# Optimization experiments

Measured on AMD Instinct MI355X. Metric: run time of the kernel, lower is better.

Reference implementation:

```python
import jax, jax.numpy as jnp
import numpy as np

N = 20000
E = 640000
IN_CH = 256
HID = 128
OUT_CH = 64
HEADS = 8
C1 = HID // HEADS   # 16 per-head dim, layer 1 (concat)
C2 = OUT_CH         # 64 per-head dim, layer 2 (head mean)
NEG_SLOPE = 0.2


def gat_conv(x, edge_index, W, a_src, a_dst, b, concat):
    """PyG GATConv (no self loops, eval mode / no dropout).
    W: [F_in, H*C], a_src/a_dst: [H, C], b: [H*C] or [C]."""
    H, C = a_src.shape
    h = (x @ W).reshape(-1, H, C)                      # [N, H, C]
    s_src = jnp.einsum('nhc,hc->nh', h, a_src)         # [N, H]
    s_dst = jnp.einsum('nhc,hc->nh', h, a_dst)         # [N, H]
    src, dst = edge_index[0], edge_index[1]
    e = jax.nn.leaky_relu(s_src[src] + s_dst[dst], NEG_SLOPE)  # [E, H]
    # segment softmax over incoming edges of each destination node
    m = jax.ops.segment_max(e, dst, num_segments=N)    # [N, H] (-inf for isolated)
    p = jnp.exp(e - m[dst])                            # [E, H]
    z = jax.ops.segment_sum(p, dst, num_segments=N)    # [N, H]
    alpha = p / z[dst]                                 # [E, H]
    out = jax.ops.segment_sum(h[src] * alpha[..., None], dst, num_segments=N)  # [N,H,C]
    out = out.reshape(-1, H * C) if concat else out.mean(axis=1)
    return out + b


def hetero_layer(x, edge_indices, Ws, a_srcs, a_dsts, bs, concat):
    # HeteroConv(aggr='mean') over edge types targeting 'user'
    outs = [gat_conv(x, edge_indices[t], Ws[t], a_srcs[t], a_dsts[t], bs[t], concat)
            for t in range(len(edge_indices))]
    return sum(outs) / len(outs)


def setup_inputs() -> dict:
    key = jax.random.key(0)
    ks = jax.random.split(key, 16)
    g = 0.1
    return {
        'x': jax.random.normal(ks[0], (N, IN_CH), dtype=jnp.float32),
        'edge_index_a': jax.random.randint(ks[1], (2, E), 0, N, dtype=jnp.int32).astype(jnp.int64),
        'edge_index_b': jax.random.randint(ks[2], (2, E), 0, N, dtype=jnp.int32).astype(jnp.int64),
        # layer 1 params, stacked over 2 edge types
        'W1': jax.random.normal(ks[3], (2, IN_CH, HEADS * C1), dtype=jnp.float32) * g,
        'a1_src': jax.random.normal(ks[4], (2, HEADS, C1), dtype=jnp.float32) * g,
        'a1_dst': jax.random.normal(ks[5], (2, HEADS, C1), dtype=jnp.float32) * g,
        'b1': jnp.zeros((2, HEADS * C1), dtype=jnp.float32),
        # layer 2 params
        'W2': jax.random.normal(ks[6], (2, HID, HEADS * C2), dtype=jnp.float32) * g,
        'a2_src': jax.random.normal(ks[7], (2, HEADS, C2), dtype=jnp.float32) * g,
        'a2_dst': jax.random.normal(ks[8], (2, HEADS, C2), dtype=jnp.float32) * g,
        'b2': jnp.zeros((2, C2), dtype=jnp.float32),
        # classifier
        'Wc1': jax.random.normal(ks[9], (OUT_CH, 32), dtype=jnp.float32) * g,
        'bc1': jnp.zeros((32,), dtype=jnp.float32),
        'Wc2': jax.random.normal(ks[10], (32, 2), dtype=jnp.float32) * g,
        'bc2': jnp.zeros((2,), dtype=jnp.float32),
    }


def reference(x, edge_index_a, edge_index_b, W1, a1_src, a1_dst, b1,
              W2, a2_src, a2_dst, b2, Wc1, bc1, Wc2, bc2):
    eis = [edge_index_a, edge_index_b]
    h = hetero_layer(x, eis, W1, a1_src, a1_dst, b1, concat=True)   # [N, 128]
    h = jax.nn.elu(h)  # (dropout is identity in eval mode)
    h = hetero_layer(h, eis, W2, a2_src, a2_dst, b2, concat=False)  # [N, 64]
    h = jax.nn.elu(h)
    logits = jax.nn.relu(h @ Wc1 + bc1) @ Wc2 + bc2                 # [N, 2]
    return logits
```

## Files before the change

kernel.cpp:

```cpp
#include <hip/hip_runtime.h>
#include <hip/hip_bf16.h>
#include <math.h>

#define NN 20000
#define EE 640000
#define NB 157
#define BCAP 5120
#define NBLK 160
#define CHNK 4000

typedef float v2f __attribute__((ext_vector_type(2)));
typedef __attribute__((ext_vector_type(8))) short bf16x8;
typedef __attribute__((ext_vector_type(4))) float f32x4;

__device__ __forceinline__ void wave_fence() {
  __builtin_amdgcn_wave_barrier();
  asm volatile("s_waitcnt lgkmcnt(0)" ::: "memory");
  __builtin_amdgcn_wave_barrier();
}

__device__ __forceinline__ unsigned pack_bf2(float a, float b) {
  __hip_bfloat162 h2 = __float22bfloat162_rn(make_float2(a, b));
  return *(unsigned*)&h2;
}
__device__ __forceinline__ float2 unpack_bf2(unsigned v) {
  float2 r;
  unsigned lo = v << 16, hi = v & 0xffff0000u;
  r.x = __uint_as_float(lo);
  r.y = __uint_as_float(hi);
  return r;
}

__global__ __launch_bounds__(256) void bin_k(const int* __restrict__ ea,
                                             const int* __restrict__ eb,
                                             int* __restrict__ gcnt,
                                             int* __restrict__ bbuf) {
  int t = blockIdx.y;
  const int* ei = t ? eb : ea;
  int tid = threadIdx.x;
  __shared__ int lh[NB], lbase[NB];
  if (tid < NB) lh[tid] = 0;
  __syncthreads();
  int e0 = blockIdx.x * CHNK;
  int e1 = min(e0 + CHNK, EE);
  int myb[16], myr[16], myv[16];
#pragma unroll
  for (int i = 0; i < 16; ++i) {
    int e = e0 + tid + i * 256;
    if (e < e1) {
      int s = ei[e], d = ei[EE + e];
      int b = d >> 7;
      myb[i] = b;
      myv[i] = (s << 7) | (d & 127);
      myr[i] = atomicAdd(&lh[b], 1);
    } else {
      myb[i] = -1;
    }
  }
  __syncthreads();
  if (tid < NB) {
    int c = lh[tid];
    lbase[tid] = c ? atomicAdd(&gcnt[t * NB + tid], c) : 0;
  }
  __syncthreads();
#pragma unroll
  for (int i = 0; i < 16; ++i) {
    int b = myb[i];
    if (b >= 0) {
      int pos = lbase[b] + myr[i];
      if (pos < BCAP) bbuf[((size_t)t * NB + b) * BCAP + pos] = myv[i];
    }
  }
}

__global__ __launch_bounds__(512) void bscan_k(const int* __restrict__ gcnt,
                                               int* __restrict__ bstart) {
  __shared__ int buf[512];
  int tid = threadIdx.x;
  int t = tid >> 8, b = tid & 255;
  int val = (b < NB) ? gcnt[t * NB + b] : 0;
  buf[tid] = val;
  __syncthreads();
  for (int s = 1; s < 256; s <<= 1) {
    int x = ((tid & 255) >= s) ? buf[tid - s] : 0;
    __syncthreads();
    buf[tid] += x;
    __syncthreads();
  }
  if (b < NB) bstart[t * NB + b] = buf[tid] - val;
}

__global__ __launch_bounds__(256) void build_k(const int* __restrict__ gcnt,
                                               const int* __restrict__ bstart,
                                               const int* __restrict__ bbuf,
                                               int* __restrict__ rowptr,
                                               int* __restrict__ csr) {
  int b = blockIdx.x, t = blockIdx.y;
  int cnt = gcnt[t * NB + b];
  int start = bstart[t * NB + b];
  int n0 = b << 7;
  int nlocal = min(128, NN - n0);
  int tid = threadIdx.x;
  __shared__ int arr[128], lcur[128];
  if (tid < 128) arr[tid] = 0;
  __syncthreads();
  const int* ebuf = bbuf + ((size_t)t * NB + b) * BCAP;
  for (int i = tid; i < cnt; i += 256) atomicAdd(&arr[ebuf[i] & 127], 1);
  __syncthreads();
  int deg = (tid < 128) ? arr[tid] : 0;
  for (int s = 1; s < 128; s <<= 1) {
    int x = (tid < 128 && tid >= s) ? arr[tid - s] : 0;
    __syncthreads();
    if (tid < 128) arr[tid] += x;
    __syncthreads();
  }
  if (tid < nlocal) {
    int incl = arr[tid];
    rowptr[t * (NN + 1) + n0 + tid + 1] = start + incl;
    lcur[tid] = start + incl - deg;
  }
  if (b == 0 && tid == 0) rowptr[t * (NN + 1)] = 0;
  __syncthreads();
  for (int i = tid; i < cnt; i += 256) {
    int v = ebuf[i];
    int pos = atomicAdd(&lcur[v & 127], 1);
    csr[(size_t)t * EE + pos] = v >> 7;
  }
}

template <int NT, int BM, int BN, int BK, int TM, int TN>
__global__ __launch_bounds__(NT) void sgemm_k(const float* __restrict__ A,
                                              const float* __restrict__ B,
                                              float* __restrict__ C, int M, int N, int K,
                                              long long Abs, long long Bbs, long long Cbs,
                                              unsigned* __restrict__ Cb, long long Cbb) {
  A += blockIdx.z * Abs; B += blockIdx.z * Bbs;
  if (C) C += blockIdx.z * Cbs;
  if (Cb) Cb += blockIdx.z * Cbb;
  const int bm = blockIdx.x * BM, bn = blockIdx.y * BN;
  __shared__ float As[BK][BM + 4];
  __shared__ float Bs[BK][BN + 4];
  int tid = threadIdx.x;
  constexpr int TX = BN / TN;
  int tx = tid % TX, ty = tid / TX;
  float acc[TM][TN] = {};
  for (int k0 = 0; k0 < K; k0 += BK) {
#pragma unroll
    for (int i = 0; i < (BM * BK) / (NT * 4); ++i) {
      int idx = tid + i * NT;
      int row = idx / (BK / 4), kq = idx % (BK / 4);
      float4 v = make_float4(0.f, 0.f, 0.f, 0.f);
      int gr = bm + row;
      if (gr < M) v = *(const float4*)&A[(size_t)gr * K + k0 + kq * 4];
      As[kq * 4 + 0][row] = v.x; As[kq * 4 + 1][row] = v.y;
      As[kq * 4 + 2][row] = v.z; As[kq * 4 + 3][row] = v.w;
    }
#pragma unroll
    for (int i = 0; i < (BK * BN) / (NT * 4); ++i) {
      int idx = tid + i * NT;
      int row = idx / (BN / 4), cq = idx % (BN / 4);
      *(float4*)&Bs[row][cq * 4] = *(const float4*)&B[(size_t)(k0 + row) * N + bn + cq * 4];
    }
    __syncthreads();
#pragma unroll
    for (int k = 0; k < BK; ++k) {
      float a[TM], b[TN];
#pragma unroll
      for (int i = 0; i < TM; i += 4) *(float4*)&a[i] = *(float4*)&As[k][ty * TM + i];
#pragma unroll
      for (int j = 0; j < TN; j += 4) *(float4*)&b[j] = *(float4*)&Bs[k][tx * TN + j];
#pragma unroll
      for (int i = 0; i < TM; ++i)
#pragma unroll
        for (int j = 0; j < TN; ++j) acc[i][j] += a[i] * b[j];
    }
    __syncthreads();
  }
#pragma unroll
  for (int i = 0; i < TM; ++i) {
    int gr = bm + ty * TM + i;
    if (gr < M) {
      if (C) {
#pragma unroll
        for (int j = 0; j < TN; j += 4)
          *(float4*)&C[(size_t)gr * N + bn + tx * TN + j] = *(float4*)&acc[i][j];
      }
      if (Cb) {
#pragma unroll
        for (int j = 0; j < TN; j += 2)
          Cb[(size_t)gr * (N >> 1) + ((bn + tx * TN + j) >> 1)] = pack_bf2(acc[i][j], acc[i][j + 1]);
      }
    }
  }
}

__global__ void scoreb_k(const unsigned* __restrict__ hb, const float* __restrict__ as_,
                         const float* __restrict__ ad_, float* __restrict__ ss,
                         float* __restrict__ sd) {
  int idx = blockIdx.x * 256 + threadIdx.x;
  if (idx >= 2 * NN * 8) return;
  int t = idx / (NN * 8), r = idx % (NN * 8), n = r / 8, hh = r % 8;
  const unsigned* hrow = hb + (size_t)t * NN * 64 + (size_t)n * 64 + hh * 8;
  const float* a1 = as_ + t * 128 + hh * 16;
  const float* a2 = ad_ + t * 128 + hh * 16;
  uint4 u0 = *(const uint4*)&hrow[0];
  uint4 u1 = *(const uint4*)&hrow[4];
  unsigned uu[8] = {u0.x, u0.y, u0.z, u0.w, u1.x, u1.y, u1.z, u1.w};
  float s1 = 0.f, s2 = 0.f;
#pragma unroll
  for (int q = 0; q < 8; ++q) {
    float2 f = unpack_bf2(uu[q]);
    s1 += f.x * a1[2 * q] + f.y * a1[2 * q + 1];
    s2 += f.x * a2[2 * q] + f.y * a2[2 * q + 1];
  }
  ss[idx] = s1; sd[idx] = s2;
}

__device__ __forceinline__ float lrelu(float v) { return v > 0.f ? v : 0.2f * v; }

__global__ __launch_bounds__(256) void aggw1_k(const int* __restrict__ rowptr,
                                               const int* __restrict__ csr,
                                               const float* __restrict__ ssrc,
                                               const float* __restrict__ sdst,
                                               const unsigned* __restrict__ hb,
                                               float* __restrict__ out) {
  int t = blockIdx.y;
  rowptr += t * (NN + 1); csr += (size_t)t * EE;
  ssrc += (size_t)t * NN * 8; sdst += (size_t)t * NN * 8;
  hb += (size_t)t * NN * 64; out += (size_t)t * NN * 128;
  int tid = threadIdx.x, w = tid >> 6, lane = tid & 63;
  int n = blockIdx.x * 4 + w;
  int row = rowptr[n], end = rowptr[n + 1];
  __shared__ __align__(16) int sidx[4][64];
  __shared__ __align__(16) float sexp[4][64][8];
  float4 sda = *(const float4*)&sdst[(size_t)n * 8];
  float4 sdb = *(const float4*)&sdst[(size_t)n * 8 + 4];
  float za_x = 0.f, za_y = 0.f, za_z = 0.f, za_w = 0.f;
  float zb_x = 0.f, zb_y = 0.f, zb_z = 0.f, zb_w = 0.f;
  int hme = lane >> 3;
  unsigned lane4 = lane << 2;
  const char* hbc = (const char*)hb;
  v2f acc = {0.f, 0.f};
  for (int base = row; base < end; base += 64) {
    int cnt = min(64, end - base);
    if (lane < cnt) {
      int s = csr[base + lane];
      sidx[w][lane] = s << 8;
      float4 pa = *(const float4*)&ssrc[(size_t)s * 8];
      float4 pb = *(const float4*)&ssrc[(size_t)s * 8 + 4];
      float4 ea, eb;
      ea.x = __expf(lrelu(pa.x + sda.x)); ea.y = __expf(lrelu(pa.y + sda.y));
      ea.z = __expf(lrelu(pa.z + sda.z)); ea.w = __expf(lrelu(pa.w + sda.w));
      eb.x = __expf(lrelu(pb.x + sdb.x)); eb.y = __expf(lrelu(pb.y + sdb.y));
      eb.z = __expf(lrelu(pb.z + sdb.z)); eb.w = __expf(lrelu(pb.w + sdb.w));
      za_x += ea.x; za_y += ea.y; za_z += ea.z; za_w += ea.w;
      zb_x += eb.x; zb_y += eb.y; zb_z += eb.z; zb_w += eb.w;
      *(float4*)&sexp[w][lane][0] = ea;
      *(float4*)&sexp[w][lane][4] = eb;
    }
    wave_fence();
    int g = 0;
    for (; g + 8 <= cnt; g += 8) {
      unsigned off[8];
      *(int4*)&off[0] = *(const int4*)&sidx[w][g];
      *(int4*)&off[4] = *(const int4*)&sidx[w][g + 4];
      unsigned uv[8];
#pragma unroll
      for (int j = 0; j < 8; ++j)
        uv[j] = *(const unsigned*)(hbc + (off[j] | lane4));
#pragma unroll
      for (int j = 0; j < 8; ++j) {
        float a = sexp[w][g + j][hme];
        float2 vf = unpack_bf2(uv[j]);
        v2f v = {vf.x, vf.y};
        acc += a * v;
      }
    }
    for (; g < cnt; ++g) {
      unsigned off = (unsigned)sidx[w][g];
      unsigned uvr = *(const unsigned*)(hbc + (off | lane4));
      float a = sexp[w][g][hme];
      float2 vf = unpack_bf2(uvr);
      v2f v = {vf.x, vf.y};
      acc += a * v;
    }
    wave_fence();
  }
#pragma unroll
  for (int off = 32; off; off >>= 1) {
    za_x += __shfl_xor(za_x, off); za_y += __shfl_xor(za_y, off);
    za_z += __shfl_xor(za_z, off); za_w += __shfl_xor(za_w, off);
    zb_x += __shfl_xor(zb_x, off); zb_y += __shfl_xor(zb_y, off);
    zb_z += __shfl_xor(zb_z, off); zb_w += __shfl_xor(zb_w, off);
  }
  float zh[8] = {za_x, za_y, za_z, za_w, zb_x, zb_y, zb_z, zb_w};
  float z = zh[hme];
  float iz = z > 0.f ? 1.f / z : 0.f;
  *(float2*)&out[(size_t)n * 128 + lane * 2] = make_float2(acc.x * iz, acc.y * iz);
}

__global__ void combine1_k(const float* __restrict__ oa, const float* __restrict__ ob,
                           const float* __restrict__ b1, float* __restrict__ hmid,
                           unsigned* __restrict__ hmidb) {
  int idx = blockIdx.x * 256 + threadIdx.x;
  if (idx >= NN * 64) return;
  int n = idx >> 6, j2 = idx & 63, j = j2 * 2;
  float2 va = *(const float2*)&oa[(size_t)n * 128 + j];
  float2 vb = *(const float2*)&ob[(size_t)n * 128 + j];
  float vx = 0.5f * ((va.x + b1[j]) + (vb.x + b1[128 + j]));
  float vy = 0.5f * ((va.y + b1[j + 1]) + (vb.y + b1[128 + j + 1]));
  vx = vx > 0.f ? vx : (__expf(vx) - 1.f);
  vy = vy > 0.f ? vy : (__expf(vy) - 1.f);
  *(float2*)&hmid[(size_t)n * 128 + j] = make_float2(vx, vy);
  hmidb[idx] = pack_bf2(vx, vy);
}

__global__ void fold2_k(const float* __restrict__ W2, const float* __restrict__ a2s,
                        const float* __restrict__ a2d, float* __restrict__ wsf,
                        float* __restrict__ wdf) {
  int idx = blockIdx.x * 256 + threadIdx.x;
  if (idx >= 2048) return;
  int t = idx >> 10, r = idx & 1023, hh = r >> 7, k = r & 127;
  const float* wrow = W2 + (size_t)t * 65536 + (size_t)k * 512 + hh * 64;
  const float* as = a2s + t * 512 + hh * 64;
  const float* ad = a2d + t * 512 + hh * 64;
  float s1 = 0.f, s2 = 0.f;
  for (int c = 0; c < 64; ++c) { s1 += wrow[c] * as[c]; s2 += wrow[c] * ad[c]; }
  wsf[idx] = s1; wdf[idx] = s2;
}

__global__ void foldBT_k(const float* __restrict__ W2, unsigned* __restrict__ BTp) {
  int idx = blockIdx.x * 256 + threadIdx.x;
  if (idx >= 65536) return;
  int t = idx >> 15, r = idx & 32767, c = r >> 9, kw = r & 511;
  int K0 = kw * 2, K1 = K0 + 1;
  int hh0 = K0 >> 7, kk0 = K0 & 127;
  int hh1 = K1 >> 7, kk1 = K1 & 127;
  float v0 = 0.125f * W2[(size_t)t * 65536 + (size_t)kk0 * 512 + hh0 * 64 + c];
  float v1 = 0.125f * W2[(size_t)t * 65536 + (size_t)kk1 * 512 + hh1 * 64 + c];
  BTp[idx] = pack_bf2(v0, v1);
}

__global__ void score2_k(const float* __restrict__ hmid, const float* __restrict__ wsf,
                         const float* __restrict__ wdf, float* __restrict__ ss,
                         float* __restrict__ sdo) {
  int idx = blockIdx.x * 256 + threadIdx.x;
  if (idx >= NN * 8) return;
  int n = idx >> 3, hh = idx & 7;
  const float* hm = hmid + (size_t)n * 128;
  const float* w0s = wsf + (size_t)hh * 128;
  const float* w0d = wdf + (size_t)hh * 128;
  const float* w1s = wsf + (size_t)(8 + hh) * 128;
  const float* w1d = wdf + (size_t)(8 + hh) * 128;
  float s0s = 0.f, s0d = 0.f, s1s = 0.f, s1d = 0.f;
#pragma unroll
  for (int c = 0; c < 128; c += 4) {
    float4 f = *(const float4*)&hm[c];
    float4 a = *(const float4*)&w0s[c];
    float4 b = *(const float4*)&w0d[c];
    float4 u = *(const float4*)&w1s[c];
    float4 v = *(const float4*)&w1d[c];
    s0s += f.x * a.x + f.y * a.y + f.z * a.z + f.w * a.w;
    s0d += f.x * b.x + f.y * b.y + f.z * b.z + f.w * b.w;
    s1s += f.x * u.x + f.y * u.y + f.z * u.z + f.w * u.w;
    s1d += f.x * v.x + f.y * v.y + f.z * v.z + f.w * v.w;
  }
  ss[idx] = s0s; sdo[idx] = s0d;
  ss[NN * 8 + idx] = s1s; sdo[NN * 8 + idx] = s1d;
}

__global__ __launch_bounds__(256) void aggw2_k(const int* __restrict__ rowptr,
                                               const int* __restrict__ csr,
                                               const float* __restrict__ ssrc,
                                               const float* __restrict__ sdst,
                                               const unsigned* __restrict__ hmidb,
                                               unsigned* __restrict__ aggp) {
  int t = blockIdx.y;
  rowptr += t * (NN + 1); csr += (size_t)t * EE;
  ssrc += (size_t)t * NN * 8; sdst += (size_t)t * NN * 8;
  aggp += (size_t)t * NN * 512;
  int tid = threadIdx.x, w = tid >> 6, lane = tid & 63;
  int n = blockIdx.x * 4 + w;
  int row = rowptr[n], end = rowptr[n + 1];
  __shared__ __align__(16) int sidx[4][64];
  __shared__ __align__(16) float sexp[4][64][8];
  float4 sda = *(const float4*)&sdst[(size_t)n * 8];
  float4 sdb = *(const float4*)&sdst[(size_t)n * 8 + 4];
  float za_x = 0.f, za_y = 0.f, za_z = 0.f, za_w = 0.f;
  float zb_x = 0.f, zb_y = 0.f, zb_z = 0.f, zb_w = 0.f;
  unsigned lane4 = lane << 2;
  const char* hbc = (const char*)hmidb;
  v2f acc[8];
#pragma unroll
  for (int i = 0; i < 8; ++i) acc[i] = (v2f){0.f, 0.f};
  for (int base = row; base < end; base += 64) {
    int cnt = min(64, end - base);
    if (lane < cnt) {
      int s = csr[base + lane];
      sidx[w][lane] = s << 8;
      float4 pa = *(const float4*)&ssrc[(size_t)s * 8];
      float4 pb = *(const float4*)&ssrc[(size_t)s * 8 + 4];
      float4 ea, eb;
      ea.x = __expf(lrelu(pa.x + sda.x)); ea.y = __expf(lrelu(pa.y + sda.y));
      ea.z = __expf(lrelu(pa.z + sda.z)); ea.w = __expf(lrelu(pa.w + sda.w));
      eb.x = __expf(lrelu(pb.x + sdb.x)); eb.y = __expf(lrelu(pb.y + sdb.y));
      eb.z = __expf(lrelu(pb.z + sdb.z)); eb.w = __expf(lrelu(pb.w + sdb.w));
      za_x += ea.x; za_y += ea.y; za_z += ea.z; za_w += ea.w;
      zb_x += eb.x; zb_y += eb.y; zb_z += eb.z; zb_w += eb.w;
      *(float4*)&sexp[w][lane][0] = ea;
      *(float4*)&sexp[w][lane][4] = eb;
    }
    wave_fence();
    int g = 0;
    for (; g + 8 <= cnt; g += 8) {
      unsigned off[8];
      *(int4*)&off[0] = *(const int4*)&sidx[w][g];
      *(int4*)&off[4] = *(const int4*)&sidx[w][g + 4];
      unsigned uv[8];
#pragma unroll
      for (int j = 0; j < 8; ++j)
        uv[j] = *(const unsigned*)(hbc + (off[j] | lane4));
#pragma unroll
      for (int j = 0; j < 8; ++j) {
        float4 ea = *(const float4*)&sexp[w][g + j][0];
        float4 eb = *(const float4*)&sexp[w][g + j][4];
        float2 vf = unpack_bf2(uv[j]);
        v2f v = {vf.x, vf.y};
        acc[0] += ea.x * v;
        acc[1] += ea.y * v;
        acc[2] += ea.z * v;
        acc[3] += ea.w * v;
        acc[4] += eb.x * v;
        acc[5] += eb.y * v;
        acc[6] += eb.z * v;
        acc[7] += eb.w * v;
      }
    }
    for (; g < cnt; ++g) {
      unsigned off = (unsigned)sidx[w][g];
      unsigned uvr = *(const unsigned*)(hbc + (off | lane4));
      float4 ea = *(const float4*)&sexp[w][g][0];
      float4 eb = *(const float4*)&sexp[w][g][4];
      float2 vf = unpack_bf2(uvr);
      v2f v = {vf.x, vf.y};
      acc[0] += ea.x * v;
      acc[1] += ea.y * v;
      acc[2] += ea.z * v;
      acc[3] += ea.w * v;
      acc[4] += eb.x * v;
      acc[5] += eb.y * v;
      acc[6] += eb.z * v;
      acc[7] += eb.w * v;
    }
    wave_fence();
  }
#pragma unroll
  for (int off = 32; off; off >>= 1) {
    za_x += __shfl_xor(za_x, off); za_y += __shfl_xor(za_y, off);
    za_z += __shfl_xor(za_z, off); za_w += __shfl_xor(za_w, off);
    zb_x += __shfl_xor(zb_x, off); zb_y += __shfl_xor(zb_y, off);
    zb_z += __shfl_xor(zb_z, off); zb_w += __shfl_xor(zb_w, off);
  }
  float zh[8] = {za_x, za_y, za_z, za_w, zb_x, zb_y, zb_z, zb_w};
#pragma unroll
  for (int i = 0; i < 8; ++i) {
    float z = zh[i];
    float iz = z > 0.f ? 1.f / z : 0.f;
    aggp[(size_t)n * 512 + i * 64 + lane] = pack_bf2(acc[i].x * iz, acc[i].y * iz);
  }
}

__global__ __launch_bounds__(256) void gemm2_k(const unsigned* __restrict__ Ap,
                                               const unsigned* __restrict__ BT,
                                               const float* __restrict__ b2,
                                               float* __restrict__ feat) {
  int tid = threadIdx.x, w = tid >> 6, l = tid & 63;
  int lr = l & 15, lgq = l >> 4;
  int rowbase = blockIdx.x * 64 + w * 16;
  int arow = rowbase + lr;
  if (arow > NN - 1) arow = NN - 1;
  f32x4 acc0 = {0.f, 0.f, 0.f, 0.f}, acc1 = acc0, acc2 = acc0, acc3 = acc0;
#pragma unroll
  for (int t = 0; t < 2; ++t) {
    const unsigned* ap = Ap + (size_t)t * NN * 512 + (size_t)arow * 512 + lgq * 4;
    const unsigned* bp = BT + t * 32768 + lr * 512 + lgq * 4;
    for (int kw = 0; kw < 512; kw += 16) {
      uint4 av = *(const uint4*)(ap + kw);
      uint4 bv0 = *(const uint4*)(bp + kw);
      uint4 bv1 = *(const uint4*)(bp + 16 * 512 + kw);
      uint4 bv2 = *(const uint4*)(bp + 32 * 512 + kw);
      uint4 bv3 = *(const uint4*)(bp + 48 * 512 + kw);
      bf16x8 afq = *(const bf16x8*)&av;
      acc0 = __builtin_amdgcn_mfma_f32_16x16x32_bf16(afq, *(const bf16x8*)&bv0, acc0, 0, 0, 0);
      acc1 = __builtin_amdgcn_mfma_f32_16x16x32_bf16(afq, *(const bf16x8*)&bv1, acc1, 0, 0, 0);
      acc2 = __builtin_amdgcn_mfma_f32_16x16x32_bf16(afq, *(const bf16x8*)&bv2, acc2, 0, 0, 0);
      acc3 = __builtin_amdgcn_mfma_f32_16x16x32_bf16(afq, *(const bf16x8*)&bv3, acc3, 0, 0, 0);
    }
  }
  f32x4 accs[4] = {acc0, acc1, acc2, acc3};
#pragma unroll
  for (int ct = 0; ct < 4; ++ct) {
    int col = ct * 16 + lr;
    float bsum = b2[col] + b2[64 + col];
#pragma unroll
    for (int r = 0; r < 4; ++r) {
      int rowq = rowbase + lgq * 4 + r;
      if (rowq < NN) {
        float v = 0.5f * (accs[ct][r] + bsum);
        v = v > 0.f ? v : (__expf(v) - 1.f);
        feat[(size_t)rowq * 64 + col] = v;
      }
    }
  }
}

__global__ __launch_bounds__(256) void cls_k(const float* __restrict__ feat,
                                             const float* __restrict__ Wc1,
                                             const float* __restrict__ bc1,
                                             const float* __restrict__ Wc2,
                                             const float* __restrict__ bc2,
                                             float* __restrict__ out) {
  __shared__ float w1[64 * 32];
  __shared__ float w2[64];
  __shared__ float b1s[32], b2s[2];
  __shared__ float fs[8 * 64];
  __shared__ float hs[8 * 32];
  int tid = threadIdx.x;
  for (int i = tid; i < 2048; i += 256) w1[i] = Wc1[i];
  if (tid < 64) w2[tid] = Wc2[tid];
  if (tid < 32) b1s[tid] = bc1[tid];
  if (tid < 2) b2s[tid] = bc2[tid];
  int nbase = blockIdx.x * 8;
  for (int i = tid; i < 512; i += 256) fs[i] = feat[(size_t)nbase * 64 + i];
  __syncthreads();
  int local = tid >> 5, tt = tid & 31;
  const float* f = fs + local * 64;
  float acc = b1s[tt];
#pragma unroll
  for (int c = 0; c < 64; ++c) acc += f[c] * w1[c * 32 + tt];
  hs[local * 32 + tt] = fmaxf(acc, 0.f);
  __syncthreads();
  if (tid < 16) {
    int l = tid >> 1, j = tid & 1;
    float o = b2s[j];
#pragma unroll
    for (int i = 0; i < 32; ++i) o += hs[l * 32 + i] * w2[i * 2 + j];
    out[(size_t)(nbase + l) * 2 + j] = o;
  }
}

extern "C" void kernel_launch(void* const* d_in, const int* in_sizes, int n_in,
                              void* d_out, int out_size, void* d_ws, size_t ws_size,
                              hipStream_t stream) {
  const float* x   = (const float*)d_in[0];
  const int* eia   = (const int*)d_in[1];
  const int* eib   = (const int*)d_in[2];
  const float* W1  = (const float*)d_in[3];
  const float* a1s = (const float*)d_in[4];
  const float* a1d = (const float*)d_in[5];
  const float* b1  = (const float*)d_in[6];
  const float* W2  = (const float*)d_in[7];
  const float* a2s = (const float*)d_in[8];
  const float* a2d = (const float*)d_in[9];
  const float* b2  = (const float*)d_in[10];
  const float* Wc1 = (const float*)d_in[11];
  const float* bc1 = (const float*)d_in[12];
  const float* Wc2 = (const float*)d_in[13];
  const float* bc2 = (const float*)d_in[14];
  float* out = (float*)d_out;

  char* ws = (char*)d_ws;
  size_t off = 0;
  auto alloc = [&](size_t bytes) -> char* {
    char* p = ws + off;
    off += (bytes + 255) & ~(size_t)255;
    return p;
  };
  int* gcnt       = (int*)alloc((size_t)2 * NB * 4);
  int* bstart     = (int*)alloc((size_t)2 * NB * 4);
  int* bbuf       = (int*)alloc((size_t)2 * NB * BCAP * 4);
  int* rowptr     = (int*)alloc((size_t)2 * (NN + 1) * 4);
  int* csr        = (int*)alloc((size_t)2 * EE * 4);
  unsigned* h1b   = (unsigned*)alloc((size_t)2 * NN * 64 * 4);
  float* s1s      = (float*)alloc((size_t)2 * NN * 8 * 4);
  float* s1d      = (float*)alloc((size_t)2 * NN * 8 * 4);
  float* o1       = (float*)alloc((size_t)2 * NN * 128 * 4);
  float* hmid     = (float*)alloc((size_t)NN * 128 * 4);
  unsigned* hmidb = (unsigned*)alloc((size_t)NN * 64 * 4);
  float* wsf      = (float*)alloc((size_t)2048 * 4);
  float* wdf      = (float*)alloc((size_t)2048 * 4);
  unsigned* BTp   = (unsigned*)alloc((size_t)65536 * 4);
  float* s2s      = (float*)alloc((size_t)2 * NN * 8 * 4);
  float* s2d      = (float*)alloc((size_t)2 * NN * 8 * 4);
  unsigned* aggp  = (unsigned*)alloc((size_t)2 * NN * 512 * 4);
  float* feat     = (float*)alloc((size_t)NN * 64 * 4);

  hipMemsetAsync(gcnt, 0, (size_t)2 * NB * 4, stream);
  bin_k<<<dim3(NBLK, 2), 256, 0, stream>>>(eia, eib, gcnt, bbuf);
  bscan_k<<<1, 512, 0, stream>>>(gcnt, bstart);
  build_k<<<dim3(NB, 2), 256, 0, stream>>>(gcnt, bstart, bbuf, rowptr, csr);

  fold2_k<<<8, 256, 0, stream>>>(W2, a2s, a2d, wsf, wdf);
  foldBT_k<<<256, 256, 0, stream>>>(W2, BTp);

  sgemm_k<256, 64, 64, 32, 4, 4><<<dim3((NN + 63) / 64, 2, 2), 256, 0, stream>>>(
      x, W1, nullptr, NN, 128, 256, 0LL, 256LL * 128, 0LL, h1b, (long long)NN * 64);
  scoreb_k<<<(2 * NN * 8 + 255) / 256, 256, 0, stream>>>(h1b, a1s, a1d, s1s, s1d);
  aggw1_k<<<dim3(NN / 4, 2), 256, 0, stream>>>(rowptr, csr, s1s, s1d, h1b, o1);
  combine1_k<<<(NN * 64 + 255) / 256, 256, 0, stream>>>(o1, o1 + (size_t)NN * 128, b1, hmid, hmidb);

  score2_k<<<(NN * 8 + 255) / 256, 256, 0, stream>>>(hmid, wsf, wdf, s2s, s2d);
  aggw2_k<<<dim3(NN / 4, 2), 256, 0, stream>>>(rowptr, csr, s2s, s2d, hmidb, aggp);
  gemm2_k<<<(NN + 63) / 64, 256, 0, stream>>>(aggp, BTp, b2, feat);

  cls_k<<<NN / 8, 256, 0, stream>>>(feat, Wc1, bc1, Wc2, bc2, out);
}
```

Baseline: 431.8 us.

## Replace layer-1 FP32 SGEMM with bf16 MFMA GEMM and shrink intermediates to bf16

The first-layer projection x@W1 moves from a scalar FP32 tiled SGEMM to a bf16 MFMA kernel. It needs two new prep kernels, one packing x to bf16 and one transposing and packing W1. The layer-1 aggregation output and the combined hidden state are now stored only as packed bf16, which halves intermediate traffic and drops the FP32 hmid buffer. score2 reads the bf16 hidden state instead. The cost is extra launches, an additional pass over x, and lower precision in intermediates.

Result: no change. 435.4 us (median of 2 runs) (+0.8%).

```diff
diff --git a/kernel.cpp b/kernel.cpp
--- a/kernel.cpp
+++ b/kernel.cpp
@@ -128,67 +128,62 @@
   }
 }
 
-template <int NT, int BM, int BN, int BK, int TM, int TN>
-__global__ __launch_bounds__(NT) void sgemm_k(const float* __restrict__ A,
-                                              const float* __restrict__ B,
-                                              float* __restrict__ C, int M, int N, int K,
-                                              long long Abs, long long Bbs, long long Cbs,
-                                              unsigned* __restrict__ Cb, long long Cbb) {
-  A += blockIdx.z * Abs; B += blockIdx.z * Bbs;
-  if (C) C += blockIdx.z * Cbs;
-  if (Cb) Cb += blockIdx.z * Cbb;
-  const int bm = blockIdx.x * BM, bn = blockIdx.y * BN;
-  __shared__ float As[BK][BM + 4];
-  __shared__ float Bs[BK][BN + 4];
-  int tid = threadIdx.x;
-  constexpr int TX = BN / TN;
-  int tx = tid % TX, ty = tid / TX;
-  float acc[TM][TN] = {};
-  for (int k0 = 0; k0 < K; k0 += BK) {
-#pragma unroll
-    for (int i = 0; i < (BM * BK) / (NT * 4); ++i) {
-      int idx = tid + i * NT;
-      int row = idx / (BK / 4), kq = idx % (BK / 4);
-      float4 v = make_float4(0.f, 0.f, 0.f, 0.f);
-      int gr = bm + row;
-      if (gr < M) v = *(const float4*)&A[(size_t)gr * K + k0 + kq * 4];
-      As[kq * 4 + 0][row] = v.x; As[kq * 4 + 1][row] = v.y;
-      As[kq * 4 + 2][row] = v.z; As[kq * 4 + 3][row] = v.w;
-    }
-#pragma unroll
-    for (int i = 0; i < (BK * BN) / (NT * 4); ++i) {
-      int idx = tid + i * NT;
-      int row = idx / (BN / 4), cq = idx % (BN / 4);
-      *(float4*)&Bs[row][cq * 4] = *(const float4*)&B[(size_t)(k0 + row) * N + bn + cq * 4];
-    }
-    __syncthreads();
-#pragma unroll
-    for (int k = 0; k < BK; ++k) {
-      float a[TM], b[TN];
-#pragma unroll
-      for (int i = 0; i < TM; i += 4) *(float4*)&a[i] = *(float4*)&As[k][ty * TM + i];
-#pragma unroll
-      for (int j = 0; j < TN; j += 4) *(float4*)&b[j] = *(float4*)&Bs[k][tx * TN + j];
-#pragma unroll
-      for (int i = 0; i < TM; ++i)
-#pragma unroll
-        for (int j = 0; j < TN; ++j) acc[i][j] += a[i] * b[j];
-    }
-    __syncthreads();
-  }
-#pragma unroll
-  for (int i = 0; i < TM; ++i) {
-    int gr = bm + ty * TM + i;
-    if (gr < M) {
-      if (C) {
-#pragma unroll
-        for (int j = 0; j < TN; j += 4)
-          *(float4*)&C[(size_t)gr * N + bn + tx * TN + j] = *(float4*)&acc[i][j];
+__global__ void packx_k(const float* __restrict__ x, unsigned* __restrict__ Xp) {
+  int idx = blockIdx.x * 256 + threadIdx.x;
+  if (idx >= NN * 128) return;
+  float2 f = *(const float2*)&x[(size_t)idx * 2];
+  Xp[idx] = pack_bf2(f.x, f.y);
+}
+
+__global__ void foldBT1_k(const float* __restrict__ W1, unsigned* __restrict__ BT1) {
+  int idx = blockIdx.x * 256 + threadIdx.x;
+  if (idx >= 32768) return;
+  int t = idx >> 14, r = idx & 16383, c = r >> 7, kw = r & 127;
+  float v0 = W1[(size_t)t * 32768 + (size_t)(2 * kw) * 128 + c];
+  float v1 = W1[(size_t)t * 32768 + (size_t)(2 * kw + 1) * 128 + c];
+  BT1[idx] = pack_bf2(v0, v1);
+}
+
+__global__ __launch_bounds__(256) void gemm1_k(const unsigned* __restrict__ Xp,
+                                               const unsigned* __restrict__ BT1,
+                                               unsigned* __restrict__ h1b) {
+  int tid = threadIdx.x, w = tid >> 6, l = tid & 63;
+  int lr = l & 15, lg = l >> 4;
+  int rowbase = blockIdx.x * 64 + w * 16;
+  int arow = rowbase + lr;
+  if (arow > NN - 1) arow = NN - 1;
+  f32x4 acc[2][8];
+#pragma unroll
+  for (int t = 0; t < 2; ++t)
+#pragma unroll
+    for (int ct = 0; ct < 8; ++ct) acc[t][ct] = (f32x4){0.f, 0.f, 0.f, 0.f};
+  const unsigned* ap = Xp + (size_t)arow * 128 + lg * 4;
+#pragma unroll
+  for (int kw = 0; kw < 128; kw += 16) {
+    uint4 av = *(const uint4*)(ap + kw);
+    bf16x8 af = *(const bf16x8*)&av;
+#pragma unroll
+    for (int t = 0; t < 2; ++t) {
+#pragma unroll
+      for (int ct = 0; ct < 8; ++ct) {
+        uint4 bv = *(const uint4*)(BT1 + (size_t)t * 16384 + (size_t)(ct * 16 + lr) * 128 + lg * 4 + kw);
+        acc[t][ct] = __builtin_amdgcn_mfma_f32_16x16x32_bf16(af, *(const bf16x8*)&bv, acc[t][ct], 0, 0, 0);
       }
-      if (Cb) {
-#pragma unroll
-        for (int j = 0; j < TN; j += 2)
-          Cb[(size_t)gr * (N >> 1) + ((bn + tx * TN + j) >> 1)] = pack_bf2(acc[i][j], acc[i][j + 1]);
+    }
+  }
+  bool wr = (l & 1) == 0;
+#pragma unroll
+  for (int t = 0; t < 2; ++t) {
+#pragma unroll
+    for (int ct = 0; ct < 8; ++ct) {
+      int col = ct * 16 + lr;
+#pragma unroll
+      for (int r = 0; r < 4; ++r) {
+        float v = acc[t][ct][r];
+        float v2 = __shfl_xor(v, 1);
+        int row = rowbase + lg * 4 + r;
+        if (wr && row < NN)
+          h1b[(size_t)t * NN * 64 + (size_t)row * 64 + (col >> 1)] = pack_bf2(v, v2);
       }
     }
   }
@@ -223,11 +218,11 @@
                                                const float* __restrict__ ssrc,
                                                const float* __restrict__ sdst,
                                                const unsigned* __restrict__ hb,
-                                               float* __restrict__ out) {
+                                               unsigned* __restrict__ out) {
   int t = blockIdx.y;
   rowptr += t * (NN + 1); csr += (size_t)t * EE;
   ssrc += (size_t)t * NN * 8; sdst += (size_t)t * NN * 8;
-  hb += (size_t)t * NN * 64; out += (size_t)t * NN * 128;
+  hb += (size_t)t * NN * 64; out += (size_t)t * NN * 64;
   int tid = threadIdx.x, w = tid >> 6, lane = tid & 63;
   int n = blockIdx.x * 4 + w;
   int row = rowptr[n], end = rowptr[n + 1];
@@ -296,22 +291,20 @@
   float zh[8] = {za_x, za_y, za_z, za_w, zb_x, zb_y, zb_z, zb_w};
   float z = zh[hme];
   float iz = z > 0.f ? 1.f / z : 0.f;
-  *(float2*)&out[(size_t)n * 128 + lane * 2] = make_float2(acc.x * iz, acc.y * iz);
-}
-
-__global__ void combine1_k(const float* __restrict__ oa, const float* __restrict__ ob,
-                           const float* __restrict__ b1, float* __restrict__ hmid,
-                           unsigned* __restrict__ hmidb) {
+  out[(size_t)n * 64 + lane] = pack_bf2(acc.x * iz, acc.y * iz);
+}
+
+__global__ void combine1_k(const unsigned* __restrict__ oa, const unsigned* __restrict__ ob,
+                           const float* __restrict__ b1, unsigned* __restrict__ hmidb) {
   int idx = blockIdx.x * 256 + threadIdx.x;
   if (idx >= NN * 64) return;
-  int n = idx >> 6, j2 = idx & 63, j = j2 * 2;
-  float2 va = *(const float2*)&oa[(size_t)n * 128 + j];
-  float2 vb = *(const float2*)&ob[(size_t)n * 128 + j];
+  int j2 = idx & 63, j = j2 * 2;
+  float2 va = unpack_bf2(oa[idx]);
+  float2 vb = unpack_bf2(ob[idx]);
   float vx = 0.5f * ((va.x + b1[j]) + (vb.x + b1[128 + j]));
   float vy = 0.5f * ((va.y + b1[j + 1]) + (vb.y + b1[128 + j + 1]));
   vx = vx > 0.f ? vx : (__expf(vx) - 1.f);
   vy = vy > 0.f ? vy : (__expf(vy) - 1.f);
-  *(float2*)&hmid[(size_t)n * 128 + j] = make_float2(vx, vy);
   hmidb[idx] = pack_bf2(vx, vy);
 }
 
@@ -341,29 +334,26 @@
   BTp[idx] = pack_bf2(v0, v1);
 }
 
-__global__ void score2_k(const float* __restrict__ hmid, const float* __restrict__ wsf,
+__global__ void score2_k(const unsigned* __restrict__ hmidb, const float* __restrict__ wsf,
                          const float* __restrict__ wdf, float* __restrict__ ss,
                          float* __restrict__ sdo) {
   int idx = blockIdx.x * 256 + threadIdx.x;
   if (idx >= NN * 8) return;
   int n = idx >> 3, hh = idx & 7;
-  const float* hm = hmid + (size_t)n * 128;
+  const unsigned* hm = hmidb + (size_t)n * 64;
   const float* w0s = wsf + (size_t)hh * 128;
   const float* w0d = wdf + (size_t)hh * 128;
   const float* w1s = wsf + (size_t)(8 + hh) * 128;
   const float* w1d = wdf + (size_t)(8 + hh) * 128;
   float s0s = 0.f, s0d = 0.f, s1s = 0.f, s1d = 0.f;
-#pragma unroll
-  for (int c = 0; c < 128; c += 4) {
-    float4 f = *(const float4*)&hm[c];
-    float4 a = *(const float4*)&w0s[c];
-    float4 b = *(const float4*)&w0d[c];
-    float4 u = *(const float4*)&w1s[c];
-    float4 v = *(const float4*)&w1d[c];
-    s0s += f.x * a.x + f.y * a.y + f.z * a.z + f.w * a.w;
-    s0d += f.x * b.x + f.y * b.y + f.z * b.z + f.w * b.w;
-    s1s += f.x * u.x + f.y * u.y + f.z * u.z + f.w * u.w;
-    s1d += f.x * v.x + f.y * v.y + f.z * v.z + f.w * v.w;
+#pragma unroll 4
+  for (int q = 0; q < 64; ++q) {
+    float2 f = unpack_bf2(hm[q]);
+    int c = 2 * q;
+    s0s += f.x * w0s[c] + f.y * w0s[c + 1];
+    s0d += f.x * w0d[c] + f.y * w0d[c + 1];
+    s1s += f.x * w1s[c] + f.y * w1s[c + 1];
+    s1d += f.x * w1d[c] + f.y * w1d[c + 1];
   }
   ss[idx] = s0s; sdo[idx] = s0d;
   ss[NN * 8 + idx] = s1s; sdo[NN * 8 + idx] = s1d;
@@ -581,11 +571,12 @@
   int* bbuf       = (int*)alloc((size_t)2 * NB * BCAP * 4);
   int* rowptr     = (int*)alloc((size_t)2 * (NN + 1) * 4);
   int* csr        = (int*)alloc((size_t)2 * EE * 4);
+  unsigned* Xp    = (unsigned*)alloc((size_t)NN * 128 * 4);
+  unsigned* BT1   = (unsigned*)alloc((size_t)32768 * 4);
   unsigned* h1b   = (unsigned*)alloc((size_t)2 * NN * 64 * 4);
   float* s1s      = (float*)alloc((size_t)2 * NN * 8 * 4);
   float* s1d      = (float*)alloc((size_t)2 * NN * 8 * 4);
-  float* o1       = (float*)alloc((size_t)2 * NN * 128 * 4);
-  float* hmid     = (float*)alloc((size_t)NN * 128 * 4);
+  unsigned* o1p   = (unsigned*)alloc((size_t)2 * NN * 64 * 4);
   unsigned* hmidb = (unsigned*)alloc((size_t)NN * 64 * 4);
   float* wsf      = (float*)alloc((size_t)2048 * 4);
   float* wdf      = (float*)alloc((size_t)2048 * 4);
@@ -602,14 +593,15 @@
 
   fold2_k<<<8, 256, 0, stream>>>(W2, a2s, a2d, wsf, wdf);
   foldBT_k<<<256, 256, 0, stream>>>(W2, BTp);
-
-  sgemm_k<256, 64, 64, 32, 4, 4><<<dim3((NN + 63) / 64, 2, 2), 256, 0, stream>>>(
-      x, W1, nullptr, NN, 128, 256, 0LL, 256LL * 128, 0LL, h1b, (long long)NN * 64);
+  foldBT1_k<<<128, 256, 0, stream>>>(W1, BT1);
+  packx_k<<<(NN * 128 + 255) / 256, 256, 0, stream>>>(x, Xp);
+
+  gemm1_k<<<(NN + 63) / 64, 256, 0, stream>>>(Xp, BT1, h1b);
   scoreb_k<<<(2 * NN * 8 + 255) / 256, 256, 0, stream>>>(h1b, a1s, a1d, s1s, s1d);
-  aggw1_k<<<dim3(NN / 4, 2), 256, 0, stream>>>(rowptr, csr, s1s, s1d, h1b, o1);
-  combine1_k<<<(NN * 64 + 255) / 256, 256, 0, stream>>>(o1, o1 + (size_t)NN * 128, b1, hmid, hmidb);
-
-  score2_k<<<(NN * 8 + 255) / 256, 256, 0, stream>>>(hmid, wsf, wdf, s2s, s2d);
+  aggw1_k<<<dim3(NN / 4, 2), 256, 0, stream>>>(rowptr, csr, s1s, s1d, h1b, o1p);
+  combine1_k<<<(NN * 64 + 255) / 256, 256, 0, stream>>>(o1p, o1p + (size_t)NN * 64, b1, hmidb);
+
+  score2_k<<<(NN * 8 + 255) / 256, 256, 0, stream>>>(hmidb, wsf, wdf, s2s, s2d);
   aggw2_k<<<dim3(NN / 4, 2), 256, 0, stream>>>(rowptr, csr, s2s, s2d, hmidb, aggp);
   gemm2_k<<<(NN + 63) / 64, 256, 0, stream>>>(aggp, BTp, b2, feat);
 
```
